# Kernel optimization log

Measured on AMD Instinct MI355X. Metric: run time of the kernel, lower is better.

## Reference

```python
import jax, jax.numpy as jnp
import numpy as np

E = 2048   # embedding_size
H = 2048   # hidden_size
B = 512    # batch
OUT = 2    # output_size (coords)


def setup_inputs() -> dict:
    key = jax.random.key(0)
    ks = jax.random.split(key, 11)
    s = 0.02
    return {
        "embedding": jax.random.normal(ks[0], (B, E), dtype=jnp.float32),
        "max_seq_length": 256,
        "W_embed": jax.random.normal(ks[1], (H, E), dtype=jnp.float32) * s,
        "b_embed": jnp.zeros((H,), dtype=jnp.float32),
        "W_ih": jax.random.normal(ks[2], (4 * H, OUT), dtype=jnp.float32) * s,
        "b_ih": jnp.zeros((4 * H,), dtype=jnp.float32),
        "W_hh": jax.random.normal(ks[3], (4 * H, H), dtype=jnp.float32) * s,
        "b_hh": jnp.zeros((4 * H,), dtype=jnp.float32),
        "W_out": jax.random.normal(ks[4], (OUT, H), dtype=jnp.float32) * s,
        "b_out": jnp.zeros((OUT,), dtype=jnp.float32),
        "W_stop": jax.random.normal(ks[5], (1, H), dtype=jnp.float32) * s,
        "b_stop": jnp.zeros((1,), dtype=jnp.float32),
    }


def reference(embedding, max_seq_length, W_embed, b_embed, W_ih, b_ih,
              W_hh, b_hh, W_out, b_out, W_stop, b_stop):
    # h_0 from embedding head (num_layers == 1)
    h0 = embedding @ W_embed.T + b_embed          # (B, H)
    c0 = jnp.zeros_like(h0)
    x0 = jnp.zeros((embedding.shape[0], OUT), dtype=embedding.dtype)

    def step(carry, _):
        h, c, x = carry
        gates = x @ W_ih.T + b_ih + h @ W_hh.T + b_hh    # (B, 4H)
        i, f, g, o = jnp.split(gates, 4, axis=-1)         # torch gate order i,f,g,o
        c = jax.nn.sigmoid(f) * c + jax.nn.sigmoid(i) * jnp.tanh(g)
        h = jax.nn.sigmoid(o) * jnp.tanh(c)
        coord = h @ W_out.T + b_out                        # (B, 2)
        stop = jax.nn.sigmoid(h @ W_stop.T + b_stop)       # (B, 1)
        return (h, c, coord), (coord, stop)

    _, (coords, stops) = jax.lax.scan(step, (h0, c0, x0), xs=None,
                                      length=max_seq_length)
    outputs = jnp.transpose(coords, (1, 0, 2))     # (B, T, 2)
    stop_probs = jnp.transpose(stops, (1, 0, 2))   # (B, T, 1)
    return outputs, stop_probs
```

## Files before the change

### kernel.cpp

```cpp
#include <hip/hip_runtime.h>
#include <stdint.h>

#define E_DIM 2048
#define H_DIM 2048
#define B_DIM 512
#define T_DIM 256
#define G4H   8192

typedef unsigned short u16;
typedef __attribute__((ext_vector_type(8))) short bf16x8;
typedef __attribute__((ext_vector_type(4))) float f32x4;

__device__ inline u16 f2b(float f) {
  union { float f; uint32_t i; } v; v.f = f;
  uint32_t u = v.i;
  return (u16)((u + 0x7FFFu + ((u >> 16) & 1u)) >> 16);
}
__device__ inline float b2f(u16 u) {
  union { uint32_t i; float f; } v; v.i = ((uint32_t)u) << 16; return v.f;
}

__device__ __forceinline__ void stage16(const void* g, void* l) {
  __builtin_amdgcn_global_load_lds(
      (const __attribute__((address_space(1))) uint32_t*)g,
      (__attribute__((address_space(3))) uint32_t*)l, 16, 0, 0);
}

__global__ __launch_bounds__(256) void convert_bf16(const float* __restrict__ s,
                                                    u16* __restrict__ d, int n4) {
  int i = blockIdx.x * 256 + threadIdx.x;
  if (i < n4) {
    float4 f = ((const float4*)s)[i];
    ushort4 o;
    o.x = f2b(f.x); o.y = f2b(f.y); o.z = f2b(f.z); o.w = f2b(f.w);
    ((ushort4*)d)[i] = o;
  }
}

__global__ __launch_bounds__(256) void build_weff(const float* __restrict__ W,
                                                  const float* __restrict__ W_ih,
                                                  const float* __restrict__ W_out,
                                                  u16* __restrict__ Wz) {
  int id = blockIdx.x * 256 + threadIdx.x;
  int lane = id & 63;
  int k32  = (id >> 6) & 63;
  int n16  = id >> 12;
  int np = n16 * 16 + (lane & 15);
  int k  = k32 * 32 + (lane >> 4) * 8;
  int g = np & 3, jrow = np >> 2;
  int src = g * H_DIM + jrow;
  float wi0 = W_ih[src * 2 + 0], wi1 = W_ih[src * 2 + 1];
  const float* sw = W + (size_t)src * H_DIM + k;
  u16 out[8];
  for (int j = 0; j < 8; ++j) {
    float v = sw[j] + wi0 * W_out[k + j] + wi1 * W_out[H_DIM + k + j];
    out[j] = f2b(v);
  }
  u16* dst = Wz + (size_t)id * 8;
  *(ushort4*)(dst) = *(ushort4*)&out[0];
  *(ushort4*)(dst + 4) = *(ushort4*)&out[4];
}

__global__ __launch_bounds__(256) void build_epi(const float* __restrict__ b_ih,
                                                 const float* __restrict__ b_hh,
                                                 const float* __restrict__ W_ih,
                                                 const float* __restrict__ b_out,
                                                 float* __restrict__ epi) {
  int np = blockIdx.x * 256 + threadIdx.x;
  int src = (np & 3) * H_DIM + (np >> 2);
  float wi0 = W_ih[src * 2 + 0], wi1 = W_ih[src * 2 + 1];
  float4 e;
  e.x = b_ih[src] + b_hh[src] + b_out[0] * wi0 + b_out[1] * wi1;
  e.y = wi0;
  e.z = wi1;
  e.w = 0.f;
  ((float4*)epi)[np] = e;
}

#define BM 64
#define BN 128
#define BK 32
__global__ __launch_bounds__(256) void gemm_bt(const u16* __restrict__ A,
                                               const u16* __restrict__ Bm,
                                               float* __restrict__ C,
                                               int M, int N, int K) {
  __shared__ u16 sA[BM * BK];
  __shared__ u16 sB[BN * BK];
  const int t = threadIdx.x;
  const int bm0 = blockIdx.y * BM, bn0 = blockIdx.x * BN;
  const int wave = t >> 6, lane = t & 63;
  const int wm = (wave >> 1) * 32, wn = (wave & 1) * 64;
  const int r16 = lane & 15, quad = lane >> 4;

  f32x4 acc[2][4];
  const f32x4 z = {0.f, 0.f, 0.f, 0.f};
  for (int i = 0; i < 2; ++i)
    for (int j = 0; j < 4; ++j) acc[i][j] = z;

  const int arow = t >> 2, acg = t & 3;

  for (int k0 = 0; k0 < K; k0 += BK) {
    __syncthreads();
    *(uint4*)&sA[arow * BK + acg * 8] =
        *(const uint4*)&A[(size_t)(bm0 + arow) * K + k0 + acg * 8];
    for (int i = 0; i < 2; ++i) {
      int c = t + 256 * i;
      int row = c >> 2, cg = c & 3;
      *(uint4*)&sB[row * BK + cg * 8] =
          *(const uint4*)&Bm[(size_t)(bn0 + row) * K + k0 + cg * 8];
    }
    __syncthreads();
    bf16x8 af[2], bfr[4];
    for (int mt = 0; mt < 2; ++mt)
      af[mt] = *(const bf16x8*)&sA[(wm + mt * 16 + r16) * BK + quad * 8];
    for (int nt = 0; nt < 4; ++nt)
      bfr[nt] = *(const bf16x8*)&sB[(wn + nt * 16 + r16) * BK + quad * 8];
    for (int mt = 0; mt < 2; ++mt)
      for (int nt = 0; nt < 4; ++nt)
        acc[mt][nt] = __builtin_amdgcn_mfma_f32_16x16x32_bf16(af[mt], bfr[nt],
                                                              acc[mt][nt], 0, 0, 0);
  }
  for (int mt = 0; mt < 2; ++mt)
    for (int nt = 0; nt < 4; ++nt) {
      int row = bm0 + wm + mt * 16 + quad * 4;
      int col = bn0 + wn + nt * 16 + r16;
      for (int r = 0; r < 4; ++r)
        C[(size_t)(row + r) * N + col] = acc[mt][nt][r];
    }
}

__global__ __launch_bounds__(256) void init_state(const float* __restrict__ h0pre,
                                                  const float* __restrict__ b_embed,
                                                  u16* __restrict__ h,
                                                  float* __restrict__ c,
                                                  float* __restrict__ xzero) {
  int idx = blockIdx.x * 256 + threadIdx.x;
  int bg = idx >> 11, k = idx & (H_DIM - 1);
  float v = h0pre[idx] + b_embed[k];
  size_t chunk = (((size_t)(bg >> 4)) * 64 + (k >> 5)) * 64 + ((k >> 3) & 3) * 16 + (bg & 15);
  size_t pos = chunk * 8 + (k & 7);
  h[pos] = f2b(v);
  c[pos] = 0.f;
  if (idx < B_DIM * 2) xzero[idx] = 0.f;
}

__global__ __launch_bounds__(64) void calc_xcorr(const float* __restrict__ h0pre,
                                                 const float* __restrict__ b_embed,
                                                 const float* __restrict__ W_out,
                                                 const float* __restrict__ b_out,
                                                 float* __restrict__ xc) {
  int m = blockIdx.x, ln = threadIdx.x;
  float s0 = 0.f, s1 = 0.f;
  for (int k = ln; k < H_DIM; k += 64) {
    float hv = h0pre[(size_t)m * H_DIM + k] + b_embed[k];
    s0 += hv * W_out[k];
    s1 += hv * W_out[H_DIM + k];
  }
  for (int off = 32; off > 0; off >>= 1) {
    s0 += __shfl_down(s0, off);
    s1 += __shfl_down(s1, off);
  }
  if (ln == 0) {
    xc[m * 2 + 0] = -(s0 + b_out[0]);
    xc[m * 2 + 1] = -(s1 + b_out[1]);
  }
}

__global__ __launch_bounds__(256) void init_out(const float* __restrict__ b_out,
                                                const float* __restrict__ b_stop,
                                                float* __restrict__ coords,
                                                float* __restrict__ stops) {
  int i = blockIdx.x * 256 + threadIdx.x;
  coords[i * 2 + 0] = b_out[0];
  coords[i * 2 + 1] = b_out[1];
  stops[i] = b_stop[0];
}

__global__ __launch_bounds__(256) void finalize_stops(float* __restrict__ stops) {
  int i = blockIdx.x * 256 + threadIdx.x;
  stops[i] = 1.f / (1.f + __expf(-stops[i]));
}

__global__ __launch_bounds__(512, 2) void gemm_lstm(const u16* __restrict__ hA,
                                                 const u16* __restrict__ Wz,
                                                 const float* __restrict__ epi,
                                                 const float* __restrict__ x,
                                                 float* __restrict__ c,
                                                 u16* __restrict__ h_out,
                                                 const float* __restrict__ W_out,
                                                 const float* __restrict__ W_stop,
                                                 float* __restrict__ coords,
                                                 float* __restrict__ stops,
                                                 int trow) {
  __shared__ __align__(16) char smem[131072];

  const int bid = blockIdx.x;
  const int nt = (bid & 7) * 8 + ((bid >> 3) & 7);
  const int mt = bid >> 6;
  const int bm0 = mt * 128;

  const int t = threadIdx.x, wv = t >> 6, ln = t & 63;
  const int kq = wv >> 2, wm = (wv >> 1) & 1, wn = wv & 1;
  const int r16 = ln & 15, quad = ln >> 4;

  const u16* gptr[8];
  uint32_t ldsoff[8];
#pragma unroll
  for (int s = 0; s < 8; ++s) {
    int ti = wv * 8 + s;
    int g = ti >> 4;
    int w = ti & 15;
    int rowi = w >> 1, kc2 = w & 1;
    int kqg = g >> 1, isB = g & 1;
    int kc = kqg * 32 + kc2;
    if (isB)
      gptr[s] = Wz + ((size_t)(nt * 8 + rowi) * 64 + kc) * 512 + ln * 8;
    else
      gptr[s] = hA + ((size_t)((bm0 >> 4) + rowi) * 64 + kc) * 512 + ln * 8;
    ldsoff[s] = (uint32_t)(kqg * 65536 + isB * 16384 + w * 1024);
  }

#pragma unroll
  for (int s = 0; s < 8; ++s) stage16(gptr[s], smem + ldsoff[s]);
#pragma unroll
  for (int s = 0; s < 8; ++s) gptr[s] += 1024;
  __syncthreads();

  f32x4 acc[4][4];
  const f32x4 z = {0.f, 0.f, 0.f, 0.f};
#pragma unroll
  for (int i = 0; i < 4; ++i)
#pragma unroll
    for (int j = 0; j < 4; ++j) acc[i][j] = z;

  const uint32_t rdbase0 = (uint32_t)(kq * 65536);

  for (int p = 0; p < 16; ++p) {
    if (p < 15) {
      const uint32_t tog = (uint32_t)(((p + 1) & 1) * 32768);
#pragma unroll
      for (int s = 0; s < 8; ++s) stage16(gptr[s], smem + (ldsoff[s] + tog));
#pragma unroll
      for (int s = 0; s < 8; ++s) gptr[s] += 1024;
    }
    const char* rb = smem + rdbase0 + (uint32_t)((p & 1) * 32768);
#pragma unroll
    for (int kc2 = 0; kc2 < 2; ++kc2) {
      bf16x8 af[4], bf[4];
#pragma unroll
      for (int i = 0; i < 4; ++i)
        af[i] = *(const bf16x8*)(rb + ((wm * 4 + i) * 2 + kc2) * 1024 + ln * 16);
#pragma unroll
      for (int i = 0; i < 4; ++i)
        bf[i] = *(const bf16x8*)(rb + 16384 + ((wn * 4 + i) * 2 + kc2) * 1024 + ln * 16);
#pragma unroll
      for (int mi = 0; mi < 4; ++mi)
#pragma unroll
        for (int ni = 0; ni < 4; ++ni)
          acc[mi][ni] = __builtin_amdgcn_mfma_f32_16x16x32_bf16(af[mi], bf[ni],
                                                                acc[mi][ni], 0, 0, 0);
    }
    __syncthreads();
  }

  float* cb = (float*)smem;
  if (kq == 1) {
    float* dst = cb + (wm * 2 + wn) * 4096;
#pragma unroll
    for (int mi = 0; mi < 4; ++mi)
#pragma unroll
      for (int ni = 0; ni < 4; ++ni)
        *(f32x4*)&dst[((mi * 4 + ni) * 64 + ln) * 4] = acc[mi][ni];
  }
  __syncthreads();
  if (kq == 0) {
    const float* src = cb + (wm * 2 + wn) * 4096;
#pragma unroll
    for (int mi = 0; mi < 4; ++mi)
#pragma unroll
      for (int ni = 0; ni < 4; ++ni)
        acc[mi][ni] += *(const f32x4*)&src[((mi * 4 + ni) * 64 + ln) * 4];
  }
  __syncthreads();

  float* gt = (float*)smem;
  if (kq == 0) {
#pragma unroll
    for (int mi = 0; mi < 4; ++mi)
#pragma unroll
      for (int ni = 0; ni < 4; ++ni) {
        int row = wm * 64 + mi * 16 + quad * 4;
        int col = wn * 64 + ni * 16 + r16;
        f32x4 v = acc[mi][ni];
#pragma unroll
        for (int r = 0; r < 4; ++r)
          gt[(row + r) * 132 + col] = v[r];
      }
  }
  __syncthreads();

  {
    const int lrow = wv * 16 + r16;
    const int bg = bm0 + lrow;
    const float x0 = x[bg * 2 + 0], x1 = x[bg * 2 + 1];
    const size_t chunk = (((size_t)(bg >> 4)) * 64 + nt) * 64 + ln;
    const int hc0 = nt * 32 + quad * 8;
    float cv[8]; u16 hv[8];
    float s0 = 0.f, s1 = 0.f, s2 = 0.f;
    const float4* epi4 = (const float4*)epi;
    f32x4 cold0 = *(const f32x4*)&c[chunk * 8 + 0];
    f32x4 cold1 = *(const f32x4*)&c[chunk * 8 + 4];
#pragma unroll
    for (int j = 0; j < 8; ++j) {
      int col = quad * 32 + j * 4;
      float4 g4 = *(const float4*)&gt[lrow * 132 + col];
      float4 e0 = epi4[nt * 128 + col + 0];
      float4 e1 = epi4[nt * 128 + col + 1];
      float4 e2 = epi4[nt * 128 + col + 2];
      float4 e3 = epi4[nt * 128 + col + 3];
      float gi = g4.x + e0.x + x0 * e0.y + x1 * e0.z;
      float gf = g4.y + e1.x + x0 * e1.y + x1 * e1.z;
      float gg = g4.z + e2.x + x0 * e2.y + x1 * e2.z;
      float go = g4.w + e3.x + x0 * e3.y + x1 * e3.z;
      float si = 1.f / (1.f + __expf(-gi));
      float sf = 1.f / (1.f + __expf(-gf));
      float so = 1.f / (1.f + __expf(-go));
      float cold = (j < 4) ? cold0[j & 3] : cold1[j & 3];
      float cn = sf * cold + si * tanhf(gg);
      cv[j] = cn;
      float hf = so * tanhf(cn);
      hv[j] = f2b(hf);
      s0 += hf * W_out[hc0 + j];
      s1 += hf * W_out[H_DIM + hc0 + j];
      s2 += hf * W_stop[hc0 + j];
    }
    *(float4*)&c[chunk * 8 + 0] = *(float4*)&cv[0];
    *(float4*)&c[chunk * 8 + 4] = *(float4*)&cv[4];
    *(ushort4*)&h_out[chunk * 8 + 0] = *(ushort4*)&hv[0];
    *(ushort4*)&h_out[chunk * 8 + 4] = *(ushort4*)&hv[4];
    s0 += __shfl_xor(s0, 16); s1 += __shfl_xor(s1, 16); s2 += __shfl_xor(s2, 16);
    s0 += __shfl_xor(s0, 32); s1 += __shfl_xor(s1, 32); s2 += __shfl_xor(s2, 32);
    if (quad == 0) {
      atomicAdd(&coords[((size_t)bg * T_DIM + trow) * 2 + 0], s0);
      atomicAdd(&coords[((size_t)bg * T_DIM + trow) * 2 + 1], s1);
      atomicAdd(&stops[(size_t)bg * T_DIM + trow], s2);
    }
  }
}

extern "C" void kernel_launch(void* const* d_in, const int* in_sizes, int n_in,
                              void* d_out, int out_size, void* d_ws, size_t ws_size,
                              hipStream_t stream) {
  const float* embedding = (const float*)d_in[0];
  const float* W_embed   = (const float*)d_in[2];
  const float* b_embed   = (const float*)d_in[3];
  const float* W_ih      = (const float*)d_in[4];
  const float* b_ih      = (const float*)d_in[5];
  const float* W_hh      = (const float*)d_in[6];
  const float* b_hh      = (const float*)d_in[7];
  const float* W_out     = (const float*)d_in[8];
  const float* b_out     = (const float*)d_in[9];
  const float* W_stop    = (const float*)d_in[10];
  const float* b_stop    = (const float*)d_in[11];

  float* coords = (float*)d_out;
  float* stops  = (float*)d_out + (size_t)B_DIM * T_DIM * 2;

  char* ws = (char*)d_ws;
  u16* W_z     = (u16*)ws;   ws += (size_t)G4H * H_DIM * 2;
  u16* W_emb_b = (u16*)ws;   ws += (size_t)H_DIM * E_DIM * 2;
  u16* emb_b   = (u16*)ws;   ws += (size_t)B_DIM * E_DIM * 2;
  float* h0pre = (float*)ws; ws += (size_t)B_DIM * H_DIM * 4;
  float* epi   = (float*)ws; ws += (size_t)G4H * 4 * 4;
  float* cbuf  = (float*)ws; ws += (size_t)B_DIM * H_DIM * 4;
  u16* hbuf0   = (u16*)ws;   ws += (size_t)B_DIM * H_DIM * 2;
  u16* hbuf1   = (u16*)ws;   ws += (size_t)B_DIM * H_DIM * 2;
  float* xcorr = (float*)ws; ws += (size_t)B_DIM * 2 * 4;
  float* xzero = (float*)ws; ws += (size_t)B_DIM * 2 * 4;

  convert_bf16<<<(B_DIM * E_DIM / 4 + 255) / 256, 256, 0, stream>>>(embedding, emb_b, B_DIM * E_DIM / 4);
  convert_bf16<<<(H_DIM * E_DIM / 4 + 255) / 256, 256, 0, stream>>>(W_embed, W_emb_b, H_DIM * E_DIM / 4);
  build_weff<<<(G4H * H_DIM / 8) / 256, 256, 0, stream>>>(W_hh, W_ih, W_out, W_z);
  build_epi<<<G4H / 256, 256, 0, stream>>>(b_ih, b_hh, W_ih, b_out, epi);
  init_out<<<(B_DIM * T_DIM) / 256, 256, 0, stream>>>(b_out, b_stop, coords, stops);

  gemm_bt<<<dim3(H_DIM / BN, B_DIM / BM), 256, 0, stream>>>(emb_b, W_emb_b, h0pre,
                                                            B_DIM, H_DIM, E_DIM);
  init_state<<<(B_DIM * H_DIM) / 256, 256, 0, stream>>>(h0pre, b_embed, hbuf0, cbuf, xzero);
  calc_xcorr<<<B_DIM, 64, 0, stream>>>(h0pre, b_embed, W_out, b_out, xcorr);

  for (int t = 0; t < T_DIM; ++t) {
    u16* h_in  = (t & 1) ? hbuf1 : hbuf0;
    u16* h_out = (t & 1) ? hbuf0 : hbuf1;
    const float* xv = (t == 0) ? xcorr : xzero;
    gemm_lstm<<<256, 512, 0, stream>>>(h_in, W_z, epi, xv, cbuf, h_out,
                                       W_out, W_stop, coords, stops, t);
  }
  finalize_stops<<<(B_DIM * T_DIM) / 256, 256, 0, stream>>>(stops);
}
```

Before: 7.217 ms.

## Replace double-buffered LDS staging with four-stage async pipeline and vmcnt waits

The per-step recurrent GEMM kernel now splits K into 32 smaller phases, staged through a four-deep ring of LDS buffers with three loads in flight. Each wave issues fewer direct-to-LDS loads per phase. Waits use explicit vmcnt counts instead of a full drain plus syncthreads. This is meant to hide global memory latency behind MFMA work. The risk is that the hand-counted waits and raw barriers must match the number of outstanding loads exactly, or the pipeline can read stale or racing LDS data.

```diff
diff --git a/kernel.cpp b/kernel.cpp
--- a/kernel.cpp
+++ b/kernel.cpp
@@ -203,28 +203,19 @@
   const int kq = wv >> 2, wm = (wv >> 1) & 1, wn = wv & 1;
   const int r16 = ln & 15, quad = ln >> 4;
 
-  const u16* gptr[8];
-  uint32_t ldsoff[8];
-#pragma unroll
-  for (int s = 0; s < 8; ++s) {
-    int ti = wv * 8 + s;
-    int g = ti >> 4;
-    int w = ti & 15;
-    int rowi = w >> 1, kc2 = w & 1;
-    int kqg = g >> 1, isB = g & 1;
-    int kc = kqg * 32 + kc2;
+  const u16* gptr[4];
+  uint32_t ldsoff[4];
+#pragma unroll
+  for (int s = 0; s < 4; ++s) {
+    int ti = wv * 4 + s;
+    int kqg = (ti >> 4) & 1, isB = (ti >> 3) & 1, rowi = ti & 7;
+    int kc0 = kqg * 32;
     if (isB)
-      gptr[s] = Wz + ((size_t)(nt * 8 + rowi) * 64 + kc) * 512 + ln * 8;
+      gptr[s] = Wz + ((size_t)(nt * 8 + rowi) * 64 + kc0) * 512 + ln * 8;
     else
-      gptr[s] = hA + ((size_t)((bm0 >> 4) + rowi) * 64 + kc) * 512 + ln * 8;
-    ldsoff[s] = (uint32_t)(kqg * 65536 + isB * 16384 + w * 1024);
-  }
-
-#pragma unroll
-  for (int s = 0; s < 8; ++s) stage16(gptr[s], smem + ldsoff[s]);
-#pragma unroll
-  for (int s = 0; s < 8; ++s) gptr[s] += 1024;
-  __syncthreads();
+      gptr[s] = hA + ((size_t)((bm0 >> 4) + rowi) * 64 + kc0) * 512 + ln * 8;
+    ldsoff[s] = (uint32_t)(kqg * 16384 + isB * 8192 + rowi * 1024);
+  }
 
   f32x4 acc[4][4];
   const f32x4 z = {0.f, 0.f, 0.f, 0.f};
@@ -233,35 +224,59 @@
 #pragma unroll
     for (int j = 0; j < 4; ++j) acc[i][j] = z;
 
-  const uint32_t rdbase0 = (uint32_t)(kq * 65536);
-
-  for (int p = 0; p < 16; ++p) {
-    if (p < 15) {
-      const uint32_t tog = (uint32_t)(((p + 1) & 1) * 32768);
-#pragma unroll
-      for (int s = 0; s < 8; ++s) stage16(gptr[s], smem + (ldsoff[s] + tog));
-#pragma unroll
-      for (int s = 0; s < 8; ++s) gptr[s] += 1024;
-    }
-    const char* rb = smem + rdbase0 + (uint32_t)((p & 1) * 32768);
-#pragma unroll
-    for (int kc2 = 0; kc2 < 2; ++kc2) {
-      bf16x8 af[4], bf[4];
-#pragma unroll
-      for (int i = 0; i < 4; ++i)
-        af[i] = *(const bf16x8*)(rb + ((wm * 4 + i) * 2 + kc2) * 1024 + ln * 16);
-#pragma unroll
-      for (int i = 0; i < 4; ++i)
-        bf[i] = *(const bf16x8*)(rb + 16384 + ((wn * 4 + i) * 2 + kc2) * 1024 + ln * 16);
-#pragma unroll
-      for (int mi = 0; mi < 4; ++mi)
-#pragma unroll
-        for (int ni = 0; ni < 4; ++ni)
-          acc[mi][ni] = __builtin_amdgcn_mfma_f32_16x16x32_bf16(af[mi], bf[ni],
-                                                                acc[mi][ni], 0, 0, 0);
-    }
-    __syncthreads();
-  }
+  const uint32_t rdbase = (uint32_t)(kq * 16384);
+
+#define STAGE_PH(pp)                                                          \
+  do {                                                                        \
+    const uint32_t _bb = ((uint32_t)(pp) & 3u) * 32768u;                      \
+    const size_t _go = (size_t)(pp) * 512;                                    \
+    _Pragma("unroll")                                                         \
+    for (int s = 0; s < 4; ++s)                                               \
+      stage16(gptr[s] + _go, smem + (_bb + ldsoff[s]));                       \
+  } while (0)
+
+#define COMPUTE_PH(pp)                                                        \
+  do {                                                                        \
+    const char* _rb = smem + ((uint32_t)(pp) & 3u) * 32768u + rdbase;         \
+    bf16x8 _af[4], _bf[4];                                                    \
+    _Pragma("unroll")                                                         \
+    for (int i = 0; i < 4; ++i)                                               \
+      _af[i] = *(const bf16x8*)(_rb + (wm * 4 + i) * 1024 + ln * 16);         \
+    _Pragma("unroll")                                                         \
+    for (int i = 0; i < 4; ++i)                                               \
+      _bf[i] = *(const bf16x8*)(_rb + 8192 + (wn * 4 + i) * 1024 + ln * 16);  \
+    _Pragma("unroll")                                                         \
+    for (int mi = 0; mi < 4; ++mi)                                            \
+      _Pragma("unroll")                                                       \
+      for (int ni = 0; ni < 4; ++ni)                                          \
+        acc[mi][ni] = __builtin_amdgcn_mfma_f32_16x16x32_bf16(                \
+            _af[mi], _bf[ni], acc[mi][ni], 0, 0, 0);                          \
+  } while (0)
+
+  STAGE_PH(0);
+  STAGE_PH(1);
+  STAGE_PH(2);
+
+#pragma unroll 4
+  for (int p = 0; p < 29; ++p) {
+    asm volatile("s_waitcnt vmcnt(8)" ::: "memory");
+    __builtin_amdgcn_s_barrier();
+    STAGE_PH(p + 3);
+    COMPUTE_PH(p);
+  }
+  asm volatile("s_waitcnt vmcnt(8)" ::: "memory");
+  __builtin_amdgcn_s_barrier();
+  COMPUTE_PH(29);
+  asm volatile("s_waitcnt vmcnt(4)" ::: "memory");
+  __builtin_amdgcn_s_barrier();
+  COMPUTE_PH(30);
+  asm volatile("s_waitcnt vmcnt(0)" ::: "memory");
+  __builtin_amdgcn_s_barrier();
+  COMPUTE_PH(31);
+  __syncthreads();
+
+#undef STAGE_PH
+#undef COMPUTE_PH
 
   float* cb = (float*)smem;
   if (kq == 1) {
```

Result: faster. 7.014 ms (-2.8%).

## Split K four ways and stream weight fragments directly into registers

Applied to the files above, without the earlier changes.

The per-step LSTM GEMM kernel now splits K across four wave groups instead of two, with each wave covering all 128 rows against 64 columns. W_hh fragments are loaded straight from global memory into double-buffered registers, so only the h activations are staged through LDS. The staging loop uses explicit vmcnt waits, raw barriers and setprio around the MFMA bursts. The aim is to cut LDS traffic and barriers per K step, at the price of twice the accumulator registers and an extra reduction round through shared memory.

```diff
diff --git a/kernel.cpp b/kernel.cpp
--- a/kernel.cpp
+++ b/kernel.cpp
@@ -197,99 +197,127 @@
   const int bid = blockIdx.x;
   const int nt = (bid & 7) * 8 + ((bid >> 3) & 7);
   const int mt = bid >> 6;
-  const int bm0 = mt * 128;
 
   const int t = threadIdx.x, wv = t >> 6, ln = t & 63;
-  const int kq = wv >> 2, wm = (wv >> 1) & 1, wn = wv & 1;
+  const int kq = wv >> 1, wn = wv & 1;
   const int r16 = ln & 15, quad = ln >> 4;
 
-  const u16* gptr[8];
-  uint32_t ldsoff[8];
+  const u16* Bb[4];
+#pragma unroll
+  for (int ni = 0; ni < 4; ++ni)
+    Bb[ni] = Wz + ((size_t)(nt * 8 + wn * 4 + ni) * 64) * 512 + ln * 8;
+  const int kbase = kq * 16;
+
+  const u16* Ag[8];
+  uint32_t Aoff[8];
 #pragma unroll
   for (int s = 0; s < 8; ++s) {
     int ti = wv * 8 + s;
-    int g = ti >> 4;
-    int w = ti & 15;
-    int rowi = w >> 1, kc2 = w & 1;
-    int kqg = g >> 1, isB = g & 1;
-    int kc = kqg * 32 + kc2;
-    if (isB)
-      gptr[s] = Wz + ((size_t)(nt * 8 + rowi) * 64 + kc) * 512 + ln * 8;
-    else
-      gptr[s] = hA + ((size_t)((bm0 >> 4) + rowi) * 64 + kc) * 512 + ln * 8;
-    ldsoff[s] = (uint32_t)(kqg * 65536 + isB * 16384 + w * 1024);
-  }
-
-#pragma unroll
-  for (int s = 0; s < 8; ++s) stage16(gptr[s], smem + ldsoff[s]);
-#pragma unroll
-  for (int s = 0; s < 8; ++s) gptr[s] += 1024;
-  __syncthreads();
-
-  f32x4 acc[4][4];
+    int kq_s = ti >> 4, kloc_s = (ti >> 3) & 1, m16i = ti & 7;
+    Ag[s] = hA + ((size_t)(mt * 8 + m16i) * 64 + kq_s * 16 + kloc_s) * 512 + ln * 8;
+    Aoff[s] = (uint32_t)(kq_s * 16384 + kloc_s * 8192 + m16i * 1024);
+  }
+
+  f32x4 acc[8][4];
   const f32x4 z = {0.f, 0.f, 0.f, 0.f};
 #pragma unroll
-  for (int i = 0; i < 4; ++i)
+  for (int i = 0; i < 8; ++i)
 #pragma unroll
     for (int j = 0; j < 4; ++j) acc[i][j] = z;
 
-  const uint32_t rdbase0 = (uint32_t)(kq * 65536);
-
-  for (int p = 0; p < 16; ++p) {
-    if (p < 15) {
-      const uint32_t tog = (uint32_t)(((p + 1) & 1) * 32768);
-#pragma unroll
-      for (int s = 0; s < 8; ++s) stage16(gptr[s], smem + (ldsoff[s] + tog));
-#pragma unroll
-      for (int s = 0; s < 8; ++s) gptr[s] += 1024;
-    }
-    const char* rb = smem + rdbase0 + (uint32_t)((p & 1) * 32768);
-#pragma unroll
-    for (int kc2 = 0; kc2 < 2; ++kc2) {
-      bf16x8 af[4], bf[4];
-#pragma unroll
-      for (int i = 0; i < 4; ++i)
-        af[i] = *(const bf16x8*)(rb + ((wm * 4 + i) * 2 + kc2) * 1024 + ln * 16);
-#pragma unroll
-      for (int i = 0; i < 4; ++i)
-        bf[i] = *(const bf16x8*)(rb + 16384 + ((wn * 4 + i) * 2 + kc2) * 1024 + ln * 16);
-#pragma unroll
-      for (int mi = 0; mi < 4; ++mi)
+#pragma unroll
+  for (int s = 0; s < 8; ++s) stage16(Ag[s], smem + Aoff[s]);
+  __builtin_amdgcn_sched_barrier(0);
+  bf16x8 bfr[2][4];
+#pragma unroll
+  for (int d = 0; d < 2; ++d)
+#pragma unroll
+    for (int ni = 0; ni < 4; ++ni)
+      bfr[d][ni] = *(const bf16x8*)(Bb[ni] + (size_t)(kbase + d) * 512);
+
+  const uint32_t ln16 = (uint32_t)(ln * 16);
+  const uint32_t rdk = (uint32_t)(kq * 16384);
+
+  for (int it = 0; it < 8; ++it) {
+    asm volatile("s_waitcnt vmcnt(8)" ::: "memory");
+    __builtin_amdgcn_s_barrier();
+    const uint32_t bb = (uint32_t)((it & 1) * 65536);
+    if (it < 7) {
+#pragma unroll
+      for (int s = 0; s < 8; ++s)
+        stage16(Ag[s] + (size_t)(it + 1) * 1024, smem + ((bb ^ 65536) + Aoff[s]));
+      __builtin_amdgcn_sched_barrier(0);
+    }
+#pragma unroll
+    for (int kloc = 0; kloc < 2; ++kloc) {
+      const char* rb = smem + bb + rdk + (uint32_t)(kloc * 8192);
+      bf16x8 af[8];
+#pragma unroll
+      for (int mi = 0; mi < 8; ++mi)
+        af[mi] = *(const bf16x8*)(rb + mi * 1024 + ln16);
+      __builtin_amdgcn_s_setprio(1);
+#pragma unroll
+      for (int mi = 0; mi < 8; ++mi)
 #pragma unroll
         for (int ni = 0; ni < 4; ++ni)
-          acc[mi][ni] = __builtin_amdgcn_mfma_f32_16x16x32_bf16(af[mi], bf[ni],
-                                                                acc[mi][ni], 0, 0, 0);
-    }
-    __syncthreads();
-  }
+          acc[mi][ni] = __builtin_amdgcn_mfma_f32_16x16x32_bf16(
+              af[mi], bfr[kloc][ni], acc[mi][ni], 0, 0, 0);
+      __builtin_amdgcn_s_setprio(0);
+      const int knext = it * 2 + kloc + 2;
+      if (knext < 16) {
+#pragma unroll
+        for (int ni = 0; ni < 4; ++ni)
+          bfr[kloc][ni] = *(const bf16x8*)(Bb[ni] + (size_t)(kbase + knext) * 512);
+      }
+    }
+  }
+  __syncthreads();
 
   float* cb = (float*)smem;
-  if (kq == 1) {
-    float* dst = cb + (wm * 2 + wn) * 4096;
-#pragma unroll
-    for (int mi = 0; mi < 4; ++mi)
+  if (kq >= 2) {
+    float* dst = cb + ((kq - 2) * 2 + wn) * 8192;
+#pragma unroll
+    for (int mi = 0; mi < 8; ++mi)
 #pragma unroll
       for (int ni = 0; ni < 4; ++ni)
         *(f32x4*)&dst[((mi * 4 + ni) * 64 + ln) * 4] = acc[mi][ni];
   }
   __syncthreads();
-  if (kq == 0) {
-    const float* src = cb + (wm * 2 + wn) * 4096;
-#pragma unroll
-    for (int mi = 0; mi < 4; ++mi)
+  if (kq < 2) {
+    const float* src = cb + (kq * 2 + wn) * 8192;
+#pragma unroll
+    for (int mi = 0; mi < 8; ++mi)
 #pragma unroll
       for (int ni = 0; ni < 4; ++ni)
         acc[mi][ni] += *(const f32x4*)&src[((mi * 4 + ni) * 64 + ln) * 4];
   }
   __syncthreads();
+  if (kq == 1) {
+    float* dst = cb + wn * 8192;
+#pragma unroll
+    for (int mi = 0; mi < 8; ++mi)
+#pragma unroll
+      for (int ni = 0; ni < 4; ++ni)
+        *(f32x4*)&dst[((mi * 4 + ni) * 64 + ln) * 4] = acc[mi][ni];
+  }
+  __syncthreads();
+  if (kq == 0) {
+    const float* src = cb + wn * 8192;
+#pragma unroll
+    for (int mi = 0; mi < 8; ++mi)
+#pragma unroll
+      for (int ni = 0; ni < 4; ++ni)
+        acc[mi][ni] += *(const f32x4*)&src[((mi * 4 + ni) * 64 + ln) * 4];
+  }
+  __syncthreads();
 
   float* gt = (float*)smem;
   if (kq == 0) {
 #pragma unroll
-    for (int mi = 0; mi < 4; ++mi)
+    for (int mi = 0; mi < 8; ++mi)
 #pragma unroll
       for (int ni = 0; ni < 4; ++ni) {
-        int row = wm * 64 + mi * 16 + quad * 4;
+        int row = mi * 16 + quad * 4;
         int col = wn * 64 + ni * 16 + r16;
         f32x4 v = acc[mi][ni];
 #pragma unroll
@@ -301,7 +329,7 @@
 
   {
     const int lrow = wv * 16 + r16;
-    const int bg = bm0 + lrow;
+    const int bg = mt * 128 + lrow;
     const float x0 = x[bg * 2 + 0], x1 = x[bg * 2 + 1];
     const size_t chunk = (((size_t)(bg >> 4)) * 64 + nt) * 64 + ln;
     const int hc0 = nt * 32 + quad * 8;
```

New measurement: 7.600 ms. 5.3% more time.
